# Kernel optimization log

Measured on AMD Instinct MI355X. Metric: run time of the kernel, lower is better.

The kernel has to match this reference:

```python
import jax, jax.numpy as jnp
import numpy as np

PATCH = 5          # patch_sz
RATE = 1           # dilation rate
W_SPATIAL = 0.1    # CX.w_spatial
SIGMA = 0.5        # CX.nn_stretch_sigma
EPS = 1e-5


def _extract_patches(x):
    # x: [N, 3, H, W] -> [N, 3*k*k, H-k+1, W-k+1] (stride 1, VALID, dilation RATE)
    return jax.lax.conv_general_dilated_patches(
        x, filter_shape=(PATCH, PATCH), window_strides=(1, 1),
        padding='VALID', rhs_dilation=(RATE, RATE))


def _cobi_cx(output, target):
    I_feat = _extract_patches(output)   # [N, C, Hf, Wf]
    T_feat = _extract_patches(target)
    N, C, Hf, Wf = T_feat.shape
    P = Hf * Wf                         # 63*63 = 3969 (== max_sampling_1d_size^2)
    I = I_feat.reshape(N, C, P)
    T = T_feat.reshape(N, C, P)
    # center both feature sets by the target mean (standard CSFlow L2 setup)
    meanT = T.mean(axis=(0, 2), keepdims=True)
    I = I - meanT
    T = T - meanT
    # pairwise squared L2 feature distances: dist[n, i, j] = ||I_ni - T_nj||^2
    r_I = jnp.sum(I * I, axis=1)                    # [N, P]
    r_T = jnp.sum(T * T, axis=1)                    # [N, P]
    A = jnp.einsum('nci,ncj->nij', I, T)            # [N, P, P]
    dist = jnp.maximum(r_I[:, :, None] + r_T[:, None, :] - 2.0 * A, 0.0)
    # CoBi spatial term: squared L2 between normalized grid coordinates
    ys, xs = jnp.meshgrid(jnp.arange(Hf), jnp.arange(Wf), indexing='ij')
    coords = jnp.stack([ys.reshape(-1) / (Hf - 1),
                        xs.reshape(-1) / (Wf - 1)], axis=0).astype(dist.dtype)  # [2, P]
    sdist = jnp.sum((coords[:, :, None] - coords[:, None, :]) ** 2, axis=0)     # [P, P]
    comb = dist + W_SPATIAL * sdist[None]           # D'_ij = D_ij + w_s * D_ij^spatial
    # relative distance -> exponential stretch -> row softmax (contextual similarity)
    d_min = jnp.min(comb, axis=2, keepdims=True)
    d_tilde = comb / (d_min + EPS)
    w = jnp.exp((1.0 - d_tilde) / SIGMA)
    cs = w / jnp.sum(w, axis=2, keepdims=True)      # [N, P, P]
    k_max = jnp.max(cs, axis=2)                     # best match per output position
    cx = jnp.mean(k_max, axis=1)                    # [N]
    return jnp.sum(-jnp.log(cx))                    # torch.sum over per-image losses


def setup_inputs() -> dict:
    key = jax.random.key(0)
    k1, k2 = jax.random.split(key)
    output = jax.random.uniform(k1, (4, 3, 67, 67), dtype=jnp.float32)
    target = jax.random.uniform(k2, (4, 3, 67, 67), dtype=jnp.float32)
    return {"output": output, "target": target}


def reference(output, target):
    return _cobi_cx(output, target)
```

## Files before the change

### kernel.cpp

```cpp
#include <hip/hip_runtime.h>
#include <hip/hip_bf16.h>
#include <math.h>

#define NB 4
#define IW 67
#define HF 63
#define PP 3969
#define PPAD 4096
#define IMGSZ (3*IW*IW)
#define C75 75
#define NSLICE 4
#define CH_PER_SL 8
#define EPSV 1e-5f
#define WSP 0.1f
#define SQ01 0.316227766016838f
#define LOG2E2 2.885390082f

#define KCH 96
#define NKG 12
#define BM 256
#define BN 128
#define TILES_I 16
#define FCH 16
#define FEAT_BLOCKS (2*NB*NKG*PPAD/256)
#define PQ_BLOCKS   (2*NB*PPAD/256)

typedef __attribute__((ext_vector_type(8))) short short8;
typedef __attribute__((ext_vector_type(4))) float f32x4;

#define OFF_PI   96
#define OFF_QJ   (96 + 16384)
#define OFF_DMIN (96 + 2*16384)
#define OFF_PART (96 + 3*16384)
#define OFF_FPART (96 + 3*16384 + 63504)
#define OFF_CNT   (OFF_FPART + 64)
#define OFF_FB    (OFF_FPART + 80)
#define FB_FLOATS (2*NB*NKG*PPAD*4)
#define NEED_BYTES ((size_t)(OFF_FB + FB_FLOATS) * 4)

#define OLD_MEAN 0
#define OLD_RI   128
#define OLD_RT   (128 + 15876)
#define OLD_DMIN (128 + 2*15876)
#define OLD_PART (128 + 3*15876)

__device__ __forceinline__ void gload_lds16(const int4* __restrict__ g, int4* l) {
    __builtin_amdgcn_global_load_lds(
        (const __attribute__((address_space(1))) void*)g,
        (__attribute__((address_space(3))) void*)l,
        16, 0, 0);
}

__global__ __launch_bounds__(256) void k_featpq(const float* __restrict__ outI,
                                                const float* __restrict__ tgtI,
                                                int4* __restrict__ fb,
                                                float* __restrict__ PiA,
                                                float* __restrict__ QjA,
                                                unsigned* __restrict__ dminU,
                                                unsigned* __restrict__ cnt) {
    int b = blockIdx.x;
    int tid = threadIdx.x;
    if (b < FEAT_BLOCKS) {
        int idx = b * 256 + tid;
        int p = idx & (PPAD - 1);
        int t = idx >> 12;
        int kg = t % NKG; int nq = t / NKG;
        int n = nq & (NB - 1); int which = nq >> 2;
        const float* img = (which ? tgtI : outI) + n * IMGSZ;
        int pcl = (p < PP) ? p : (PP - 1);
        int py = pcl / HF, px = pcl - py * HF;
        const float* base = img + py * IW + px;
        unsigned us[8];
        #pragma unroll
        for (int e = 0; e < 8; ++e) {
            int ch = kg * 8 + e;
            float v;
            if (ch < C75) {
                int c = ch / 25, rem = ch - c * 25, ky = rem / 5, kx = rem - ky * 5;
                v = base[(c * IW + ky) * IW + kx];
            } else if (ch == 75) v = SQ01 * (float)py * (1.f / 62.f);
            else if (ch == 76)   v = SQ01 * (float)px * (1.f / 62.f);
            else v = 0.f;
            __hip_bfloat16 h = __float2bfloat16(v);
            us[e] = *reinterpret_cast<unsigned short*>(&h);
        }
        int4 o;
        o.x = (int)(us[0] | (us[1] << 16));
        o.y = (int)(us[2] | (us[3] << 16));
        o.z = (int)(us[4] | (us[5] << 16));
        o.w = (int)(us[6] | (us[7] << 16));
        fb[idx] = o;
    } else {
        int idx = (b - FEAT_BLOCKS) * 256 + tid;
        if (idx == 0) atomicExch(cnt, 0u);
        int p = idx & (PPAD - 1);
        int nq = idx >> 12; int n = nq & (NB - 1); int which = nq >> 2;
        float* dst = (which ? QjA : PiA) + n * PPAD + p;
        if (p >= PP) { *dst = which ? 1e30f : 0.f; return; }
        if (!which) dminU[n * PP + p] = 0x7f800000u;
        int py = p / HF, px = p - py * HF;
        float cy = (float)py * (1.f / 62.f), cx = (float)px * (1.f / 62.f);
        float s = WSP * (cy * cy + cx * cx);
        const float* img = (which ? tgtI : outI) + n * IMGSZ + py * IW + px;
        #pragma unroll
        for (int c = 0; c < 3; ++c)
            #pragma unroll
            for (int ky = 0; ky < 5; ++ky)
                #pragma unroll
                for (int kx = 0; kx < 5; ++kx) {
                    float v = img[(c * IW + ky) * IW + kx];
                    s = fmaf(v, v, s);
                }
        *dst = s;
    }
}

template<int PASS>
__global__ __launch_bounds__(512, 2) void k_pass(const int4* __restrict__ fb,
                                                 const float* __restrict__ PiA,
                                                 const float* __restrict__ QjA,
                                                 unsigned* __restrict__ dminU,
                                                 float* __restrict__ part) {
    __shared__ __align__(16) int4 lB[2][NKG * BN];
    __shared__ float red[2 * BM];

    const int tid = threadIdx.x;
    const int it = blockIdx.x, sl = blockIdx.y, n = blockIdx.z;
    const int i0 = it * BM;
    const int wid = tid >> 6, lane = tid & 63;
    const int wr = wid >> 1, wc = wid & 1;
    const int g = lane >> 4, c16 = lane & 15;

    const int4* fbA = fb + (size_t)(n * NKG) * PPAD;
    const int4* fbB = fb + (size_t)((NB + n) * NKG) * PPAD;

    short8 af[3][4];
    #pragma unroll
    for (int ks = 0; ks < 3; ++ks)
        #pragma unroll
        for (int mf = 0; mf < 4; ++mf)
            af[ks][mf] = *reinterpret_cast<const short8*>(
                &fbA[(ks * 4 + g) * PPAD + i0 + wr * 64 + mf * 16 + c16]);

    float rmin[16], racc[16], slope[16], c0[16];
    #pragma unroll
    for (int mf = 0; mf < 4; ++mf)
        #pragma unroll
        for (int r = 0; r < 4; ++r) {
            int q = mf * 4 + r;
            rmin[q] = 1e30f; racc[q] = 0.f;
            if (PASS == 2) {
                int i = i0 + wr * 64 + mf * 16 + g * 4 + r;
                int ic = (i < PP) ? i : (PP - 1);
                float u = LOG2E2 / (__uint_as_float(dminU[n * PP + ic]) + EPSV);
                slope[q] = 2.f * u;
                c0[q] = fmaf(-u, PiA[n * PPAD + i], LOG2E2);
            }
        }

    const int seg0 = wid * 3;
    {
        const int j0 = (sl * CH_PER_SL) * BN;
        #pragma unroll
        for (int s2 = 0; s2 < 3; ++s2) {
            int idx = (seg0 + s2) * 64 + lane;
            int kg = idx >> 7, col = idx & 127;
            gload_lds16(&fbB[kg * PPAD + j0 + col], &lB[0][(seg0 + s2) * 64]);
        }
    }
    __syncthreads();

    int cur = 0;
    for (int ch = 0; ch < CH_PER_SL; ++ch) {
        const int j0 = (sl * CH_PER_SL + ch) * BN;
        if (ch + 1 < CH_PER_SL) {
            const int j1 = j0 + BN;
            #pragma unroll
            for (int s2 = 0; s2 < 3; ++s2) {
                int idx = (seg0 + s2) * 64 + lane;
                int kg = idx >> 7, col = idx & 127;
                gload_lds16(&fbB[kg * PPAD + j1 + col], &lB[cur ^ 1][(seg0 + s2) * 64]);
            }
        }
        float qj[4];
        #pragma unroll
        for (int nf = 0; nf < 4; ++nf)
            qj[nf] = QjA[n * PPAD + j0 + wc * 64 + nf * 16 + c16];

        f32x4 acc[4][4];
        #pragma unroll
        for (int mf = 0; mf < 4; ++mf)
            #pragma unroll
            for (int nf = 0; nf < 4; ++nf)
                acc[mf][nf] = (f32x4)(0.f);

        #pragma unroll
        for (int ks = 0; ks < 3; ++ks) {
            short8 bfr[4];
            #pragma unroll
            for (int nf = 0; nf < 4; ++nf)
                bfr[nf] = *reinterpret_cast<const short8*>(
                    &lB[cur][(ks * 4 + g) * BN + wc * 64 + nf * 16 + c16]);
            #pragma unroll
            for (int mf = 0; mf < 4; ++mf)
                #pragma unroll
                for (int nf = 0; nf < 4; ++nf)
                    acc[mf][nf] = __builtin_amdgcn_mfma_f32_16x16x32_bf16(af[ks][mf], bfr[nf], acc[mf][nf], 0, 0, 0);
        }

        if (PASS == 1) {
            #pragma unroll
            for (int nf = 0; nf < 4; ++nf)
                #pragma unroll
                for (int mf = 0; mf < 4; ++mf)
                    #pragma unroll
                    for (int r = 0; r < 4; ++r) {
                        int q = mf * 4 + r;
                        rmin[q] = fminf(rmin[q], fmaf(-2.f, acc[mf][nf][r], qj[nf]));
                    }
        } else {
            #pragma unroll
            for (int nf = 0; nf < 4; ++nf) {
                float qjh = -0.5f * qj[nf];
                float bq[16];
                #pragma unroll
                for (int q = 0; q < 16; ++q)
                    bq[q] = fmaf(slope[q], qjh, c0[q]);
                #pragma unroll
                for (int mf = 0; mf < 4; ++mf)
                    #pragma unroll
                    for (int r = 0; r < 4; ++r) {
                        int q = mf * 4 + r;
                        racc[q] += __builtin_amdgcn_exp2f(fmaf(slope[q], acc[mf][nf][r], bq[q]));
                    }
            }
        }
        __syncthreads();
        cur ^= 1;
    }

    #pragma unroll
    for (int q = 0; q < 16; ++q) {
        float v = (PASS == 1) ? rmin[q] : racc[q];
        #pragma unroll
        for (int m = 1; m <= 8; m <<= 1) {
            float o = __shfl_xor(v, m);
            v = (PASS == 1) ? fminf(v, o) : (v + o);
        }
        if (c16 == 0) {
            int mf = q >> 2, r = q & 3;
            red[wc * BM + wr * 64 + mf * 16 + g * 4 + r] = v;
        }
    }
    __syncthreads();
    if (tid < BM) {
        int i = i0 + tid;
        if (i < PP) {
            if (PASS == 1) {
                float v = fminf(red[tid], red[BM + tid]) + PiA[n * PPAD + i];
                atomicMin(dminU + n * PP + i, __float_as_uint(v));
            } else {
                part[(n * NSLICE + sl) * PP + i] = red[tid] + red[BM + tid];
            }
        }
    }
}

__global__ __launch_bounds__(256) void k_fin(const unsigned* __restrict__ dminU,
                                             const float* __restrict__ part,
                                             float* __restrict__ fpart,
                                             unsigned* __restrict__ cnt,
                                             float* __restrict__ out) {
    __shared__ float red[256];
    __shared__ int lastFlag;
    int b = blockIdx.x;
    int n = b >> 4, c = b & 15;
    int tid = threadIdx.x;
    int i = c * 256 + tid;
    float v = 0.f;
    if (i < PP) {
        float dm = __uint_as_float(dminU[n * PP + i]);
        float inv = 1.f / (dm + EPSV);
        float num = __expf(2.f * (1.f - dm * inv));
        float S = part[(n * NSLICE + 0) * PP + i] + part[(n * NSLICE + 1) * PP + i]
                + part[(n * NSLICE + 2) * PP + i] + part[(n * NSLICE + 3) * PP + i];
        v = num / S;
    }
    red[tid] = v; __syncthreads();
    for (int w = 128; w > 0; w >>= 1) { if (tid < w) red[tid] += red[tid + w]; __syncthreads(); }
    if (tid == 0) {
        atomicExch(&fpart[b], red[0]);
        __threadfence();
        unsigned old = atomicAdd(cnt, 1u);
        lastFlag = (old == (unsigned)(NB * FCH - 1));
    }
    __syncthreads();
    if (lastFlag && tid < 64) {
        __threadfence();
        float s = atomicAdd(&fpart[tid], 0.f);
        s += __shfl_xor(s, 1);
        s += __shfl_xor(s, 2);
        s += __shfl_xor(s, 4);
        s += __shfl_xor(s, 8);
        float s0 = __shfl(s, 0);
        float s1 = __shfl(s, 16);
        float s2 = __shfl(s, 32);
        float s3 = __shfl(s, 48);
        if (tid == 0) {
            const float invP = 1.f / (float)PP;
            out[0] = -(__logf(s0 * invP) + __logf(s1 * invP)
                     + __logf(s2 * invP) + __logf(s3 * invP));
        }
    }
}

__global__ void k_init(unsigned* __restrict__ dminU) {
    int g = blockIdx.x * 256 + threadIdx.x;
    if (g < NB * PP) dminU[g] = 0x7f800000u;
}

__global__ __launch_bounds__(256) void k_mean(const float* __restrict__ tgt,
                                              float* __restrict__ meanv) {
    __shared__ float red[256];
    int c75 = blockIdx.x;
    int c = c75 / 25, rem = c75 - c * 25, ky = rem / 5, kx = rem - ky * 5;
    int tid = threadIdx.x;
    float s = 0.f;
    for (int idx = tid; idx < NB * PP; idx += 256) {
        int n = idx / PP, p = idx - n * PP;
        int py = p / HF, px = p - py * HF;
        s += tgt[n * IMGSZ + (c * IW + py + ky) * IW + px + kx];
    }
    red[tid] = s; __syncthreads();
    for (int w = 128; w > 0; w >>= 1) { if (tid < w) red[tid] += red[tid + w]; __syncthreads(); }
    if (tid == 0) meanv[c75] = red[0] * (1.f / (float)(NB * PP));
}

__global__ __launch_bounds__(256) void k_rsqF(const float* __restrict__ outI,
                                              const float* __restrict__ tgtI,
                                              const float* __restrict__ meanv,
                                              float* __restrict__ rI, float* __restrict__ rT) {
    int gidx = blockIdx.x * 256 + threadIdx.x;
    if (gidx >= 2 * NB * PP) return;
    int which = gidx / (NB * PP); int rem = gidx - which * NB * PP;
    int n = rem / PP, p = rem - n * PP;
    int py = p / HF, px = p - py * HF;
    const float* img = (which ? tgtI : outI) + n * IMGSZ;
    float s = 0.f;
    #pragma unroll
    for (int c = 0; c < 3; ++c)
        #pragma unroll
        for (int ky = 0; ky < 5; ++ky)
            #pragma unroll
            for (int kx = 0; kx < 5; ++kx) {
                float v = img[(c * IW + py + ky) * IW + px + kx] - meanv[(c * 5 + ky) * 5 + kx];
                s = fmaf(v, v, s);
            }
    (which ? rT : rI)[n * PP + p] = s;
}

__device__ __forceinline__ void stage_featF(const float* __restrict__ img,
                                            const float* __restrict__ meanv,
                                            float* __restrict__ lds, int p0, int tid) {
    for (int idx = tid; idx < C75 * 128; idx += 256) {
        int c75 = idx >> 7, col = idx & 127;
        int p = p0 + col; p = (p < PP) ? p : (PP - 1);
        int py = p / HF, px = p - py * HF;
        int c = c75 / 25, rem = c75 - c * 25, ky = rem / 5, kx = rem - ky * 5;
        lds[idx] = img[(c * IW + py + ky) * IW + px + kx] - meanv[c75];
    }
}

template<int PASS>
__global__ __launch_bounds__(256, 2) void k_passF(const float* __restrict__ outI,
                                                  const float* __restrict__ tgtI,
                                                  const float* __restrict__ meanv,
                                                  const float* __restrict__ rI,
                                                  const float* __restrict__ rT,
                                                  unsigned* __restrict__ dminU,
                                                  float* __restrict__ part) {
    __shared__ __align__(16) float lA[C75 * 128];
    __shared__ __align__(16) float lB[C75 * 128];
    __shared__ float red[4 * 128];
    __shared__ float lrT[128];

    const int tid = threadIdx.x;
    const int it = blockIdx.x, sl = blockIdx.y, n = blockIdx.z;
    const int i0 = it * 128;
    const int ti4 = (tid & 15) * 4;
    const int tj4 = (tid >> 4) * 4;

    stage_featF(outI + n * IMGSZ, meanv, lA, i0, tid);

    int lr[8]; float iyn[8], ixn[8], rIr[8], invr[8];
    #pragma unroll
    for (int r = 0; r < 8; ++r) {
        lr[r] = (r < 4) ? (ti4 + r) : (64 + ti4 + (r - 4));
        int i = i0 + lr[r]; int ic = (i < PP) ? i : (PP - 1);
        int iy = ic / HF, ix = ic - iy * HF;
        iyn[r] = (float)iy / 62.f; ixn[r] = (float)ix / 62.f;
        rIr[r] = rI[n * PP + ic];
        if (PASS == 2) {
            float dm = __uint_as_float(dminU[n * PP + ic]);
            invr[r] = 1.f / (dm + EPSV);
        }
    }

    float raccF[8];
    #pragma unroll
    for (int r = 0; r < 8; ++r) raccF[r] = (PASS == 1) ? 3.0e38f : 0.f;

    for (int ch = 0; ch < CH_PER_SL; ++ch) {
        const int j0 = (sl * CH_PER_SL + ch) * 128;
        __syncthreads();
        stage_featF(tgtI + n * IMGSZ, meanv, lB, j0, tid);
        if (tid < 128) {
            int j = j0 + tid;
            lrT[tid] = rT[n * PP + ((j < PP) ? j : (PP - 1))];
        }
        __syncthreads();

        float jyn[8], jxn[8], rTr[8]; bool jok[8];
        #pragma unroll
        for (int s = 0; s < 8; ++s) {
            int jc = (s < 4) ? (tj4 + s) : (64 + tj4 + (s - 4));
            int j = j0 + jc;
            jok[s] = (j < PP);
            int jcl = jok[s] ? j : (PP - 1);
            int jy = jcl / HF, jx = jcl - jy * HF;
            jyn[s] = (float)jy / 62.f; jxn[s] = (float)jx / 62.f;
            rTr[s] = lrT[jc];
        }

        float acc[8][8];
        #pragma unroll
        for (int r = 0; r < 8; ++r)
            #pragma unroll
            for (int s = 0; s < 8; ++s) acc[r][s] = 0.f;

        #pragma unroll 3
        for (int c = 0; c < C75; ++c) {
            const float4 a0 = *reinterpret_cast<const float4*>(lA + c * 128 + ti4);
            const float4 a1 = *reinterpret_cast<const float4*>(lA + c * 128 + 64 + ti4);
            const float4 b0 = *reinterpret_cast<const float4*>(lB + c * 128 + tj4);
            const float4 b1 = *reinterpret_cast<const float4*>(lB + c * 128 + 64 + tj4);
            const float av[8] = {a0.x, a0.y, a0.z, a0.w, a1.x, a1.y, a1.z, a1.w};
            const float bv[8] = {b0.x, b0.y, b0.z, b0.w, b1.x, b1.y, b1.z, b1.w};
            #pragma unroll
            for (int r = 0; r < 8; ++r)
                #pragma unroll
                for (int s = 0; s < 8; ++s)
                    acc[r][s] = fmaf(av[r], bv[s], acc[r][s]);
        }

        #pragma unroll
        for (int r = 0; r < 8; ++r) {
            #pragma unroll
            for (int s = 0; s < 8; ++s) {
                float d = rIr[r] + rTr[s] - 2.f * acc[r][s];
                d = fmaxf(d, 0.f);
                float dy = iyn[r] - jyn[s], dx = ixn[r] - jxn[s];
                float comb = d + WSP * (dy * dy + dx * dx);
                if (PASS == 1) {
                    raccF[r] = fminf(raccF[r], jok[s] ? comb : 3.0e38f);
                } else {
                    float w = __expf(2.f * (1.f - comb * invr[r]));
                    raccF[r] += jok[s] ? w : 0.f;
                }
            }
        }
    }

    const int wv = tid >> 6;
    const bool wrt = ((tid >> 4) & 3) == 0;
    #pragma unroll
    for (int r = 0; r < 8; ++r) {
        float v = raccF[r];
        if (PASS == 1) {
            v = fminf(v, __shfl_xor(v, 16));
            v = fminf(v, __shfl_xor(v, 32));
        } else {
            v += __shfl_xor(v, 16);
            v += __shfl_xor(v, 32);
        }
        if (wrt) red[wv * 128 + lr[r]] = v;
    }
    __syncthreads();
    if (tid < 128) {
        int i = i0 + tid;
        if (i < PP) {
            if (PASS == 1) {
                float v = fminf(fminf(red[tid], red[128 + tid]),
                                fminf(red[256 + tid], red[384 + tid]));
                atomicMin(dminU + n * PP + i, __float_as_uint(v));
            } else {
                float v = red[tid] + red[128 + tid] + red[256 + tid] + red[384 + tid];
                part[(n * NSLICE + sl) * PP + i] = v;
            }
        }
    }
}

__global__ __launch_bounds__(256) void k_finF(const unsigned* __restrict__ dminU,
                                              const float* __restrict__ part,
                                              float* __restrict__ out) {
    __shared__ float red[256];
    int tid = threadIdx.x;
    float loss = 0.f;
    for (int n = 0; n < NB; ++n) {
        float local = 0.f;
        for (int i = tid; i < PP; i += 256) {
            float dm = __uint_as_float(dminU[n * PP + i]);
            float inv = 1.f / (dm + EPSV);
            float num = __expf(2.f * (1.f - dm * inv));
            float S = part[(n * NSLICE + 0) * PP + i] + part[(n * NSLICE + 1) * PP + i]
                    + part[(n * NSLICE + 2) * PP + i] + part[(n * NSLICE + 3) * PP + i];
            local += num / S;
        }
        red[tid] = local; __syncthreads();
        for (int w = 128; w > 0; w >>= 1) { if (tid < w) red[tid] += red[tid + w]; __syncthreads(); }
        if (tid == 0) loss -= __logf(red[0] * (1.f / (float)PP));
        __syncthreads();
    }
    if (tid == 0) out[0] = loss;
}

extern "C" void kernel_launch(void* const* d_in, const int* in_sizes, int n_in,
                              void* d_out, int out_size, void* d_ws, size_t ws_size,
                              hipStream_t stream) {
    const float* outI = (const float*)d_in[0];
    const float* tgtI = (const float*)d_in[1];
    float* ws = (float*)d_ws;
    float* outp = (float*)d_out;

    if (ws_size >= NEED_BYTES) {
        float* PiA = ws + OFF_PI;
        float* QjA = ws + OFF_QJ;
        unsigned* dminU = (unsigned*)(ws + OFF_DMIN);
        float* part = ws + OFF_PART;
        float* fpart = ws + OFF_FPART;
        unsigned* cnt = (unsigned*)(ws + OFF_CNT);
        int4* fb = (int4*)(ws + OFF_FB);

        k_featpq<<<FEAT_BLOCKS + PQ_BLOCKS, 256, 0, stream>>>(outI, tgtI, fb, PiA, QjA, dminU, cnt);
        dim3 g(TILES_I, NSLICE, NB);
        k_pass<1><<<g, 512, 0, stream>>>(fb, PiA, QjA, dminU, part);
        k_pass<2><<<g, 512, 0, stream>>>(fb, PiA, QjA, dminU, part);
        k_fin<<<NB * FCH, 256, 0, stream>>>(dminU, part, fpart, cnt, outp);
    } else {
        float* meanv = ws + OLD_MEAN;
        float* rI = ws + OLD_RI;
        float* rT = ws + OLD_RT;
        unsigned* dminU = (unsigned*)(ws + OLD_DMIN);
        float* part = ws + OLD_PART;

        k_init<<<(NB * PP + 255) / 256, 256, 0, stream>>>(dminU);
        k_mean<<<C75, 256, 0, stream>>>(tgtI, meanv);
        k_rsqF<<<(2 * NB * PP + 255) / 256, 256, 0, stream>>>(outI, tgtI, meanv, rI, rT);
        dim3 g(32, NSLICE, NB);
        k_passF<1><<<g, 256, 0, stream>>>(outI, tgtI, meanv, rI, rT, dminU, part);
        k_passF<2><<<g, 256, 0, stream>>>(outI, tgtI, meanv, rI, rT, dminU, part);
        k_finF<<<1, 256, 0, stream>>>(dminU, part, outp);
    }
}
```

Measured before the change: 50.44 us.

## Fuse all stages into one cooperative persistent kernel with grid syncs

Replaces the four separate launches (feature/norm prep, min pass, exp-sum pass, final reduction) with a single cooperative kernel of 256 blocks that uses grid.sync between stages, keeping the A-fragments in registers across both passes. The aim is to remove the launch gaps and the repeated A-operand loads between kernels. In exchange it adds grid-wide barriers, uses 512-thread blocks for the prep phase, and limits occupancy to a grid that must fit co-resident. The old multi-kernel path is kept as a fallback if the cooperative launch fails.

```diff
diff --git a/kernel.cpp b/kernel.cpp
--- a/kernel.cpp
+++ b/kernel.cpp
@@ -1,6 +1,9 @@
 #include <hip/hip_runtime.h>
+#include <hip/hip_cooperative_groups.h>
 #include <hip/hip_bf16.h>
 #include <math.h>
+
+namespace cg = cooperative_groups;
 
 #define NB 4
 #define IW 67
@@ -21,7 +24,6 @@
 #define BM 256
 #define BN 128
 #define TILES_I 16
-#define FCH 16
 #define FEAT_BLOCKS (2*NB*NKG*PPAD/256)
 #define PQ_BLOCKS   (2*NB*PPAD/256)
 
@@ -49,6 +51,325 @@
         (const __attribute__((address_space(1))) void*)g,
         (__attribute__((address_space(3))) void*)l,
         16, 0, 0);
+}
+
+__global__ __launch_bounds__(512, 2) void k_all(const float* __restrict__ outI,
+                                                const float* __restrict__ tgtI,
+                                                int4* __restrict__ fb,
+                                                float* __restrict__ PiA,
+                                                float* __restrict__ QjA,
+                                                unsigned* __restrict__ dminU,
+                                                float* __restrict__ part,
+                                                float* __restrict__ fpart,
+                                                unsigned* __restrict__ cnt,
+                                                float* __restrict__ out) {
+    cg::grid_group grid = cg::this_grid();
+    __shared__ __align__(16) int4 lB[2][NKG * BN];
+    __shared__ float red[2 * BM];
+    __shared__ int lastFlag;
+
+    const int tid = threadIdx.x;
+    const int bid = blockIdx.x;
+
+    for (int idx = bid * 512 + tid; idx < 2 * NB * NKG * PPAD; idx += 256 * 512) {
+        int p = idx & (PPAD - 1);
+        int t = idx >> 12;
+        int kg = t % NKG; int nq = t / NKG;
+        int n = nq & (NB - 1); int which = nq >> 2;
+        const float* img = (which ? tgtI : outI) + n * IMGSZ;
+        int pcl = (p < PP) ? p : (PP - 1);
+        int py = pcl / HF, px = pcl - py * HF;
+        const float* base = img + py * IW + px;
+        unsigned us[8];
+        #pragma unroll
+        for (int e = 0; e < 8; ++e) {
+            int ch = kg * 8 + e;
+            float v;
+            if (ch < C75) {
+                int c = ch / 25, rem = ch - c * 25, ky = rem / 5, kx = rem - ky * 5;
+                v = base[(c * IW + ky) * IW + kx];
+            } else if (ch == 75) v = SQ01 * (float)py * (1.f / 62.f);
+            else if (ch == 76)   v = SQ01 * (float)px * (1.f / 62.f);
+            else v = 0.f;
+            __hip_bfloat16 h = __float2bfloat16(v);
+            us[e] = *reinterpret_cast<unsigned short*>(&h);
+        }
+        int4 o;
+        o.x = (int)(us[0] | (us[1] << 16));
+        o.y = (int)(us[2] | (us[3] << 16));
+        o.z = (int)(us[4] | (us[5] << 16));
+        o.w = (int)(us[6] | (us[7] << 16));
+        fb[idx] = o;
+    }
+    for (int idx = bid * 512 + tid; idx < 2 * NB * PPAD; idx += 256 * 512) {
+        if (idx == 0) atomicExch(cnt, 0u);
+        int p = idx & (PPAD - 1);
+        int nq = idx >> 12; int n = nq & (NB - 1); int which = nq >> 2;
+        float* dst = (which ? QjA : PiA) + n * PPAD + p;
+        if (p >= PP) { *dst = which ? 1e30f : 0.f; continue; }
+        if (!which) dminU[n * PP + p] = 0x7f800000u;
+        int py = p / HF, px = p - py * HF;
+        float cy = (float)py * (1.f / 62.f), cx = (float)px * (1.f / 62.f);
+        float s = WSP * (cy * cy + cx * cx);
+        const float* img = (which ? tgtI : outI) + n * IMGSZ + py * IW + px;
+        #pragma unroll
+        for (int c = 0; c < 3; ++c)
+            #pragma unroll
+            for (int ky = 0; ky < 5; ++ky)
+                #pragma unroll
+                for (int kx = 0; kx < 5; ++kx) {
+                    float v = img[(c * IW + ky) * IW + kx];
+                    s = fmaf(v, v, s);
+                }
+        *dst = s;
+    }
+    grid.sync();
+
+    const int it = bid & 15, sl = (bid >> 4) & 3, n = bid >> 6;
+    const int i0 = it * BM;
+    const int wid = tid >> 6, lane = tid & 63;
+    const int wr = wid >> 1, wc = wid & 1;
+    const int g = lane >> 4, c16 = lane & 15;
+    const int seg0 = wid * 3;
+    const int4* fbA = fb + (size_t)(n * NKG) * PPAD;
+    const int4* fbB = fb + (size_t)((NB + n) * NKG) * PPAD;
+
+    short8 af[3][4];
+    #pragma unroll
+    for (int ks = 0; ks < 3; ++ks)
+        #pragma unroll
+        for (int mf = 0; mf < 4; ++mf)
+            af[ks][mf] = *reinterpret_cast<const short8*>(
+                &fbA[(ks * 4 + g) * PPAD + i0 + wr * 64 + mf * 16 + c16]);
+
+    {
+        float rmin[16];
+        #pragma unroll
+        for (int q = 0; q < 16; ++q) rmin[q] = 1e30f;
+
+        {
+            const int j0 = (sl * CH_PER_SL) * BN;
+            #pragma unroll
+            for (int s2 = 0; s2 < 3; ++s2) {
+                int idx = (seg0 + s2) * 64 + lane;
+                int kg = idx >> 7, col = idx & 127;
+                gload_lds16(&fbB[kg * PPAD + j0 + col], &lB[0][(seg0 + s2) * 64]);
+            }
+        }
+        __syncthreads();
+
+        int cur = 0;
+        for (int ch = 0; ch < CH_PER_SL; ++ch) {
+            const int j0 = (sl * CH_PER_SL + ch) * BN;
+            if (ch + 1 < CH_PER_SL) {
+                const int j1 = j0 + BN;
+                #pragma unroll
+                for (int s2 = 0; s2 < 3; ++s2) {
+                    int idx = (seg0 + s2) * 64 + lane;
+                    int kg = idx >> 7, col = idx & 127;
+                    gload_lds16(&fbB[kg * PPAD + j1 + col], &lB[cur ^ 1][(seg0 + s2) * 64]);
+                }
+            }
+            float qj[4];
+            #pragma unroll
+            for (int nf = 0; nf < 4; ++nf)
+                qj[nf] = QjA[n * PPAD + j0 + wc * 64 + nf * 16 + c16];
+
+            f32x4 acc[4][4];
+            #pragma unroll
+            for (int mf = 0; mf < 4; ++mf)
+                #pragma unroll
+                for (int nf = 0; nf < 4; ++nf)
+                    acc[mf][nf] = (f32x4)(0.f);
+
+            #pragma unroll
+            for (int ks = 0; ks < 3; ++ks) {
+                short8 bfr[4];
+                #pragma unroll
+                for (int nf = 0; nf < 4; ++nf)
+                    bfr[nf] = *reinterpret_cast<const short8*>(
+                        &lB[cur][(ks * 4 + g) * BN + wc * 64 + nf * 16 + c16]);
+                #pragma unroll
+                for (int mf = 0; mf < 4; ++mf)
+                    #pragma unroll
+                    for (int nf = 0; nf < 4; ++nf)
+                        acc[mf][nf] = __builtin_amdgcn_mfma_f32_16x16x32_bf16(af[ks][mf], bfr[nf], acc[mf][nf], 0, 0, 0);
+            }
+
+            #pragma unroll
+            for (int nf = 0; nf < 4; ++nf)
+                #pragma unroll
+                for (int mf = 0; mf < 4; ++mf)
+                    #pragma unroll
+                    for (int r = 0; r < 4; ++r) {
+                        int q = mf * 4 + r;
+                        rmin[q] = fminf(rmin[q], fmaf(-2.f, acc[mf][nf][r], qj[nf]));
+                    }
+            __syncthreads();
+            cur ^= 1;
+        }
+
+        #pragma unroll
+        for (int q = 0; q < 16; ++q) {
+            float v = rmin[q];
+            #pragma unroll
+            for (int m = 1; m <= 8; m <<= 1) v = fminf(v, __shfl_xor(v, m));
+            if (c16 == 0) {
+                int mf = q >> 2, r = q & 3;
+                red[wc * BM + wr * 64 + mf * 16 + g * 4 + r] = v;
+            }
+        }
+        __syncthreads();
+        if (tid < BM) {
+            int i = i0 + tid;
+            if (i < PP) {
+                float v = fminf(red[tid], red[BM + tid]) + PiA[n * PPAD + i];
+                atomicMin(dminU + n * PP + i, __float_as_uint(v));
+            }
+        }
+    }
+    grid.sync();
+
+    {
+        float racc[16], slope[16], c0[16];
+        #pragma unroll
+        for (int mf = 0; mf < 4; ++mf)
+            #pragma unroll
+            for (int r = 0; r < 4; ++r) {
+                int q = mf * 4 + r;
+                racc[q] = 0.f;
+                int i = i0 + wr * 64 + mf * 16 + g * 4 + r;
+                int ic = (i < PP) ? i : (PP - 1);
+                float u = LOG2E2 / (__uint_as_float(dminU[n * PP + ic]) + EPSV);
+                slope[q] = 2.f * u;
+                c0[q] = fmaf(-u, PiA[n * PPAD + i], LOG2E2);
+            }
+
+        {
+            const int j0 = (sl * CH_PER_SL) * BN;
+            #pragma unroll
+            for (int s2 = 0; s2 < 3; ++s2) {
+                int idx = (seg0 + s2) * 64 + lane;
+                int kg = idx >> 7, col = idx & 127;
+                gload_lds16(&fbB[kg * PPAD + j0 + col], &lB[0][(seg0 + s2) * 64]);
+            }
+        }
+        __syncthreads();
+
+        int cur = 0;
+        for (int ch = 0; ch < CH_PER_SL; ++ch) {
+            const int j0 = (sl * CH_PER_SL + ch) * BN;
+            if (ch + 1 < CH_PER_SL) {
+                const int j1 = j0 + BN;
+                #pragma unroll
+                for (int s2 = 0; s2 < 3; ++s2) {
+                    int idx = (seg0 + s2) * 64 + lane;
+                    int kg = idx >> 7, col = idx & 127;
+                    gload_lds16(&fbB[kg * PPAD + j1 + col], &lB[cur ^ 1][(seg0 + s2) * 64]);
+                }
+            }
+            float qj[4];
+            #pragma unroll
+            for (int nf = 0; nf < 4; ++nf)
+                qj[nf] = QjA[n * PPAD + j0 + wc * 64 + nf * 16 + c16];
+
+            f32x4 acc[4][4];
+            #pragma unroll
+            for (int mf = 0; mf < 4; ++mf)
+                #pragma unroll
+                for (int nf = 0; nf < 4; ++nf)
+                    acc[mf][nf] = (f32x4)(0.f);
+
+            #pragma unroll
+            for (int ks = 0; ks < 3; ++ks) {
+                short8 bfr[4];
+                #pragma unroll
+                for (int nf = 0; nf < 4; ++nf)
+                    bfr[nf] = *reinterpret_cast<const short8*>(
+                        &lB[cur][(ks * 4 + g) * BN + wc * 64 + nf * 16 + c16]);
+                #pragma unroll
+                for (int mf = 0; mf < 4; ++mf)
+                    #pragma unroll
+                    for (int nf = 0; nf < 4; ++nf)
+                        acc[mf][nf] = __builtin_amdgcn_mfma_f32_16x16x32_bf16(af[ks][mf], bfr[nf], acc[mf][nf], 0, 0, 0);
+            }
+
+            #pragma unroll
+            for (int nf = 0; nf < 4; ++nf) {
+                float qjh = -0.5f * qj[nf];
+                float bq[16];
+                #pragma unroll
+                for (int q = 0; q < 16; ++q)
+                    bq[q] = fmaf(slope[q], qjh, c0[q]);
+                #pragma unroll
+                for (int mf = 0; mf < 4; ++mf)
+                    #pragma unroll
+                    for (int r = 0; r < 4; ++r) {
+                        int q = mf * 4 + r;
+                        racc[q] += __builtin_amdgcn_exp2f(fmaf(slope[q], acc[mf][nf][r], bq[q]));
+                    }
+            }
+            __syncthreads();
+            cur ^= 1;
+        }
+
+        #pragma unroll
+        for (int q = 0; q < 16; ++q) {
+            float v = racc[q];
+            #pragma unroll
+            for (int m = 1; m <= 8; m <<= 1) v += __shfl_xor(v, m);
+            if (c16 == 0) {
+                int mf = q >> 2, r = q & 3;
+                red[wc * BM + wr * 64 + mf * 16 + g * 4 + r] = v;
+            }
+        }
+        __syncthreads();
+        if (tid < BM) {
+            int i = i0 + tid;
+            if (i < PP)
+                part[(n * NSLICE + sl) * PP + i] = red[tid] + red[BM + tid];
+        }
+    }
+    grid.sync();
+
+    if (bid < 32) {
+        int nD = bid >> 3, cD = bid & 7;
+        int i = cD * 512 + tid;
+        float v = 0.f;
+        if (i < PP) {
+            float dm = __uint_as_float(dminU[nD * PP + i]);
+            float inv = 1.f / (dm + EPSV);
+            float num = __expf(2.f * (1.f - dm * inv));
+            float S = part[(nD * NSLICE + 0) * PP + i] + part[(nD * NSLICE + 1) * PP + i]
+                    + part[(nD * NSLICE + 2) * PP + i] + part[(nD * NSLICE + 3) * PP + i];
+            v = num / S;
+        }
+        red[tid] = v; __syncthreads();
+        for (int w = 256; w > 0; w >>= 1) { if (tid < w) red[tid] += red[tid + w]; __syncthreads(); }
+        if (tid == 0) {
+            atomicExch(&fpart[bid], red[0]);
+            __threadfence();
+            unsigned old = atomicAdd(cnt, 1u);
+            lastFlag = (old == 31u);
+        }
+        __syncthreads();
+        if (lastFlag && tid < 64) {
+            __threadfence();
+            float s = (tid < 32) ? atomicAdd(&fpart[tid], 0.f) : 0.f;
+            s += __shfl_xor(s, 1);
+            s += __shfl_xor(s, 2);
+            s += __shfl_xor(s, 4);
+            float s0 = __shfl(s, 0);
+            float s1 = __shfl(s, 8);
+            float s2 = __shfl(s, 16);
+            float s3 = __shfl(s, 24);
+            if (tid == 0) {
+                const float invP = 1.f / (float)PP;
+                out[0] = -(__logf(s0 * invP) + __logf(s1 * invP)
+                         + __logf(s2 * invP) + __logf(s3 * invP));
+            }
+        }
+    }
 }
 
 __global__ __launch_bounds__(256) void k_featpq(const float* __restrict__ outI,
@@ -292,7 +613,7 @@
         atomicExch(&fpart[b], red[0]);
         __threadfence();
         unsigned old = atomicAdd(cnt, 1u);
-        lastFlag = (old == (unsigned)(NB * FCH - 1));
+        lastFlag = (old == 63u);
     }
     __syncthreads();
     if (lastFlag && tid < 64) {
@@ -542,11 +863,18 @@
         unsigned* cnt = (unsigned*)(ws + OFF_CNT);
         int4* fb = (int4*)(ws + OFF_FB);
 
-        k_featpq<<<FEAT_BLOCKS + PQ_BLOCKS, 256, 0, stream>>>(outI, tgtI, fb, PiA, QjA, dminU, cnt);
-        dim3 g(TILES_I, NSLICE, NB);
-        k_pass<1><<<g, 512, 0, stream>>>(fb, PiA, QjA, dminU, part);
-        k_pass<2><<<g, 512, 0, stream>>>(fb, PiA, QjA, dminU, part);
-        k_fin<<<NB * FCH, 256, 0, stream>>>(dminU, part, fpart, cnt, outp);
+        void* args[] = { (void*)&outI, (void*)&tgtI, (void*)&fb, (void*)&PiA,
+                         (void*)&QjA, (void*)&dminU, (void*)&part, (void*)&fpart,
+                         (void*)&cnt, (void*)&outp };
+        hipError_t e = hipLaunchCooperativeKernel((const void*)k_all, dim3(256), dim3(512),
+                                                  args, 0, stream);
+        if (e != hipSuccess) {
+            k_featpq<<<FEAT_BLOCKS + PQ_BLOCKS, 256, 0, stream>>>(outI, tgtI, fb, PiA, QjA, dminU, cnt);
+            dim3 g(TILES_I, NSLICE, NB);
+            k_pass<1><<<g, 512, 0, stream>>>(fb, PiA, QjA, dminU, part);
+            k_pass<2><<<g, 512, 0, stream>>>(fb, PiA, QjA, dminU, part);
+            k_fin<<<64, 256, 0, stream>>>(dminU, part, fpart, cnt, outp);
+        }
     } else {
         float* meanv = ws + OLD_MEAN;
         float* rI = ws + OLD_RI;
```

Result: slower. 146.2 us (+189.9%).
